# Kernel optimization log

Hardware: AMD Instinct MI355X
Metric: run time of the kernel (lower is better)

The kernel has to match this reference:

```python
import jax, jax.numpy as jnp
import numpy as np

B, S, D = 4, 2048, 768   # batch, seq_len, dim_inp
H, E = 12, 64            # num_heads, dim_out (per-head)
LN_EPS = 1e-5


def setup_inputs() -> dict:
    key = jax.random.key(0)
    ks = jax.random.split(key, 12)
    sd = 1.0 / np.sqrt(D)
    x = jax.random.normal(ks[0], (B, S, D), dtype=jnp.float32)
    Wq = jax.random.normal(ks[1], (H, D, E), dtype=jnp.float32) * sd
    bq = jax.random.normal(ks[2], (H, E), dtype=jnp.float32) * 0.02
    Wk = jax.random.normal(ks[3], (H, D, E), dtype=jnp.float32) * sd
    bk = jax.random.normal(ks[4], (H, E), dtype=jnp.float32) * 0.02
    Wv = jax.random.normal(ks[5], (H, D, E), dtype=jnp.float32) * sd
    bv = jax.random.normal(ks[6], (H, E), dtype=jnp.float32) * 0.02
    Wo = jax.random.normal(ks[7], (H * E, D), dtype=jnp.float32) * (1.0 / np.sqrt(H * E))
    bo = jax.random.normal(ks[8], (D,), dtype=jnp.float32) * 0.02
    gamma = jnp.ones((D,), dtype=jnp.float32)
    beta = jnp.zeros((D,), dtype=jnp.float32)
    return {"input_tensor": x, "Wq": Wq, "bq": bq, "Wk": Wk, "bk": bk,
            "Wv": Wv, "bv": bv, "Wo": Wo, "bo": bo, "gamma": gamma, "beta": beta}


def reference(input_tensor, Wq, bq, Wk, bk, Wv, bv, Wo, bo, gamma, beta):
    x = input_tensor  # [B,S,D]
    # all heads at once: [B,H,S,E]
    q = jnp.einsum('bsd,hde->bhse', x, Wq) + bq[None, :, None, :]
    k = jnp.einsum('bsd,hde->bhse', x, Wk) + bk[None, :, None, :]
    v = jnp.einsum('bsd,hde->bhse', x, Wv) + bv[None, :, None, :]
    # NOTE: original divides by sqrt(seq_len) (query.size(1)), not sqrt(head_dim)
    scale = jnp.sqrt(jnp.float32(q.shape[2]))
    scores = jnp.einsum('bhse,bhte->bhst', q, k) / scale  # [B,H,S,S]
    attn = jax.nn.softmax(scores, axis=-1)
    ctx = jnp.einsum('bhst,bhte->bhse', attn, v)          # [B,H,S,E]
    # concat heads along last dim: [B,S,H*E]
    ctx = ctx.transpose(0, 2, 1, 3).reshape(x.shape[0], x.shape[1], -1)
    proj = ctx @ Wo + bo                                   # [B,S,D]
    h = x + proj
    mu = jnp.mean(h, axis=-1, keepdims=True)
    var = jnp.mean(jnp.square(h - mu), axis=-1, keepdims=True)
    y = (h - mu) * jax.lax.rsqrt(var + LN_EPS) * gamma + beta
    return y
```

## Files before the change

kernel.cpp:

```cpp
#include <hip/hip_runtime.h>


typedef __bf16 bf16x8 __attribute__((ext_vector_type(8)));
typedef __bf16 bf16x4 __attribute__((ext_vector_type(4)));
typedef float  f32x4  __attribute__((ext_vector_type(4)));
typedef float  f32x16 __attribute__((ext_vector_type(16)));
typedef unsigned u32x4 __attribute__((ext_vector_type(4)));

#define MFMA16(a,b,c) __builtin_amdgcn_mfma_f32_16x16x32_bf16((a),(b),(c),0,0,0)
#define MFMA32(a,b,c) __builtin_amdgcn_mfma_f32_32x32x16_bf16((a),(b),(c),0,0,0)
#define QSCALE2 (0.022097086912079612f * 1.4426950408889634f)

__device__ __forceinline__ void gload16(const void* g, void* l) {
  __builtin_amdgcn_global_load_lds((const __attribute__((address_space(1))) void*)g,
                                   (__attribute__((address_space(3))) void*)l, 16, 0, 0);
}

__global__ __launch_bounds__(256) void pack_kernel(
    const float* __restrict__ x, const float* __restrict__ Wq,
    const float* __restrict__ Wk, const float* __restrict__ Wv,
    const float* __restrict__ Wo,
    __bf16* __restrict__ xb, __bf16* __restrict__ wqkv, __bf16* __restrict__ wot) {
  int tid = blockIdx.x * 256 + threadIdx.x;
  int nth = gridDim.x * 256;
  for (int i = tid; i < 8192 * 768 / 4; i += nth) {
    float4 v = ((const float4*)x)[i];
    bf16x4 o; o[0] = (__bf16)v.x; o[1] = (__bf16)v.y; o[2] = (__bf16)v.z; o[3] = (__bf16)v.w;
    ((bf16x4*)xb)[i] = o;
  }
  for (int i = tid; i < 3 * 768 * 768; i += nth) {
    int n = i / 768, d = i - n * 768;
    int p = n / 768;
    int wn = n - p * 768;
    int h = wn >> 6, e = wn & 63;
    const float* W = (p == 0) ? Wq : (p == 1) ? Wk : Wv;
    wqkv[i] = (__bf16)W[(h * 768 + d) * 64 + e];
  }
  for (int i = tid; i < 768 * 768; i += nth) {
    int n = i / 768, k = i - n * 768;
    wot[i] = (__bf16)Wo[k * 768 + n];
  }
}

#define GEMM_CORE(A_, Bt_, m0_, n0_)                                              \
  __shared__ __bf16 As[128 * 32];                                                 \
  __shared__ __bf16 Bs[128 * 32];                                                 \
  const int tid = threadIdx.x;                                                    \
  const int w = tid >> 6, lane = tid & 63, ln = lane & 15, hi = lane >> 4;        \
  const int wr = w >> 1, wc = w & 1;                                              \
  f32x4 acc[4][4];                                                                \
  {                                                                               \
    f32x4 z = {0.f, 0.f, 0.f, 0.f};                                               \
    _Pragma("unroll") for (int i = 0; i < 4; ++i)                                 \
      _Pragma("unroll") for (int j = 0; j < 4; ++j) acc[i][j] = z;                \
  }                                                                               \
  {                                                                               \
    const int r0 = tid >> 2, cc = (tid & 3) * 8;                                  \
    const __bf16* ga0 = A_ + (size_t)(m0_ + r0) * 768 + cc;                       \
    const __bf16* ga1 = A_ + (size_t)(m0_ + 64 + r0) * 768 + cc;                  \
    const __bf16* gb0 = Bt_ + (size_t)(n0_ + r0) * 768 + cc;                      \
    const __bf16* gb1 = Bt_ + (size_t)(n0_ + 64 + r0) * 768 + cc;                 \
    __bf16* la0 = &As[w * 512];                                                   \
    __bf16* la1 = &As[2048 + w * 512];                                            \
    __bf16* lb0 = &Bs[w * 512];                                                   \
    __bf16* lb1 = &Bs[2048 + w * 512];                                            \
    for (int kt = 0; kt < 24; ++kt) {                                             \
      const int kk = kt * 32;                                                     \
      gload16(ga0 + kk, la0);                                                     \
      gload16(ga1 + kk, la1);                                                     \
      gload16(gb0 + kk, lb0);                                                     \
      gload16(gb1 + kk, lb1);                                                     \
      __syncthreads();                                                            \
      bf16x8 af[4], bfv[4];                                                       \
      _Pragma("unroll") for (int mt = 0; mt < 4; ++mt)                            \
        af[mt] = *(const bf16x8*)&As[(wr * 64 + mt * 16 + ln) * 32 + hi * 8];     \
      _Pragma("unroll") for (int nt = 0; nt < 4; ++nt)                            \
        bfv[nt] = *(const bf16x8*)&Bs[(wc * 64 + nt * 16 + ln) * 32 + hi * 8];    \
      _Pragma("unroll") for (int mt = 0; mt < 4; ++mt)                            \
        _Pragma("unroll") for (int nt = 0; nt < 4; ++nt)                          \
          acc[mt][nt] = MFMA16(af[mt], bfv[nt], acc[mt][nt]);                     \
      __syncthreads();                                                            \
    }                                                                             \
  }

__global__ __launch_bounds__(256) void gemm_qkv(
    const __bf16* __restrict__ A, const __bf16* __restrict__ Bt,
    const float* __restrict__ bq, const float* __restrict__ bk,
    const float* __restrict__ bv,
    __bf16* __restrict__ qb, __bf16* __restrict__ kb, __bf16* __restrict__ vt) {
  const int lin = blockIdx.y * 18 + blockIdx.x;
  const int swzb = (lin & 7) * 144 + (lin >> 3);
  const int m0 = (swzb / 18) * 128, n0 = (swzb % 18) * 128;
  GEMM_CORE(A, Bt, m0, n0)
  const int p = n0 / 768;
  const float* bias = (p == 0) ? bq : (p == 1) ? bk : bv;
  const float sc = (p == 0) ? QSCALE2 : 1.0f;
#pragma unroll
  for (int nt = 0; nt < 4; ++nt) {
    int n = n0 + wc * 64 + nt * 16 + ln;
    int wn = n - p * 768;
    int h = wn >> 6, e = wn & 63;
    float bb = bias[wn];
#pragma unroll
    for (int mt = 0; mt < 4; ++mt) {
      int mrow = m0 + wr * 64 + mt * 16 + hi * 4;
      int b = mrow >> 11, s0 = mrow & 2047;
      if (p == 2) {
        bf16x4 pk;
#pragma unroll
        for (int r = 0; r < 4; ++r) pk[r] = (__bf16)(acc[mt][nt][r] + bb);
        *(bf16x4*)&vt[(((size_t)b * 12 + h) * 64 + e) * 2048 + s0] = pk;
      } else {
        __bf16* dst = (p == 0) ? qb : kb;
#pragma unroll
        for (int r = 0; r < 4; ++r)
          dst[(((size_t)b * 12 + h) * 2048 + s0 + r) * 64 + e] =
              (__bf16)((acc[mt][nt][r] + bb) * sc);
      }
    }
  }
}

__global__ __launch_bounds__(256) void gemm_proj(
    const __bf16* __restrict__ A, const __bf16* __restrict__ Bt,
    const float* __restrict__ bo, const float* __restrict__ xres,
    float* __restrict__ hout) {
  const int lin = blockIdx.y * 6 + blockIdx.x;
  const int swzb = (lin & 7) * 48 + (lin >> 3);
  const int m0 = (swzb / 6) * 128, n0 = (swzb % 6) * 128;
  GEMM_CORE(A, Bt, m0, n0)
#pragma unroll
  for (int nt = 0; nt < 4; ++nt) {
    int n = n0 + wc * 64 + nt * 16 + ln;
    float bb = bo[n];
#pragma unroll
    for (int mt = 0; mt < 4; ++mt) {
      int mrow = m0 + wr * 64 + mt * 16 + hi * 4;
#pragma unroll
      for (int r = 0; r < 4; ++r) {
        size_t idx = (size_t)(mrow + r) * 768 + n;
        hout[idx] = acc[mt][nt][r] + bb + xres[idx];
      }
    }
  }
}

__global__ __launch_bounds__(256, 3) void attn_kernel(
    const __bf16* __restrict__ qb, const __bf16* __restrict__ kb,
    const __bf16* __restrict__ vt, __bf16* __restrict__ ctx) {
  __shared__ __align__(16) char lds[32768];
  const int tid = threadIdx.x;
  const int w = tid >> 6, lane = tid & 63;
  const int l31 = lane & 31, h = lane >> 5;
  const int bh = blockIdx.x;
  const int q0 = blockIdx.y * 128 + w * 32;

  const int o0 = tid * 16, o1 = o0 + 4096;
  const int r0s = o0 >> 7, cb0 = o0 & 127;
  const int r1s = o1 >> 7, cb1 = o1 & 127;
  const char* kgb = (const char*)(kb + (size_t)bh * 2048 * 64);
  const char* vgb = (const char*)(vt + (size_t)bh * 64 * 2048);
  const char* ksrc0 = kgb + r0s * 128 + (cb0 ^ ((r0s & 7) << 4));
  const char* ksrc1 = kgb + r1s * 128 + (cb1 ^ ((r1s & 7) << 4));
  const char* vsrc0 = vgb + r0s * 4096 + (cb0 ^ ((r0s & 7) << 4));
  const char* vsrc1 = vgb + r1s * 4096 + (cb1 ^ ((r1s & 7) << 4));
  char* kl0 = lds + w * 1024;
  char* vl0 = lds + 16384 + w * 1024;

#define STAGE(t_, b_) do {                                   \
    gload16(ksrc0 + (size_t)(t_) * 8192, kl0 + (b_) * 8192); \
    gload16(ksrc1 + (size_t)(t_) * 8192, kl0 + (b_) * 8192 + 4096); \
    gload16(vsrc0 + (size_t)(t_) * 128,  vl0 + (b_) * 8192); \
    gload16(vsrc1 + (size_t)(t_) * 128,  vl0 + (b_) * 8192 + 4096); \
  } while (0)

  const __bf16* qp = qb + ((size_t)bh * 2048 + q0 + l31) * 64 + h * 8;
  bf16x8 qf[4];
#pragma unroll
  for (int s = 0; s < 4; ++s) qf[s] = *(const bf16x8*)(qp + 16 * s);

  const int swz = (l31 & 7) << 4;
  const int krd = l31 * 128 + ((h * 16) ^ swz);
  const int vrd = 16384 + l31 * 128 + ((h * 16) ^ swz);
  int ka_[8], va_[8];
#pragma unroll
  for (int kvt = 0; kvt < 2; ++kvt)
#pragma unroll
    for (int s = 0; s < 4; ++s) ka_[kvt * 4 + s] = (krd + kvt * 4096) ^ (s * 32);
#pragma unroll
  for (int ks = 0; ks < 4; ++ks)
#pragma unroll
    for (int et = 0; et < 2; ++et) va_[ks * 2 + et] = (vrd + et * 4096) ^ (ks * 32);

  f32x16 FZ;
#pragma unroll
  for (int r = 0; r < 16; ++r) FZ[r] = 0.f;
  bf16x8 onesf;
#pragma unroll
  for (int j = 0; j < 8; ++j) onesf[j] = (__bf16)1.0f;

  f32x16 lacc = FZ;
  f32x16 cacc[2];
  cacc[0] = FZ; cacc[1] = FZ;

  STAGE(0, 0);
  __syncthreads();

#define PKPAIR(dst_, i_)                                                       \
  {                                                                            \
    float pa_ = __builtin_amdgcn_exp2f(sa[2 * (i_)]);                          \
    float pb_ = __builtin_amdgcn_exp2f(sa[2 * (i_) + 1]);                      \
    asm("v_cvt_pk_bf16_f32 %0, %1, %2" : "=v"(dst_) : "v"(pa_), "v"(pb_));     \
  }

#define TILEBODY(B_, T_)                                                       \
  {                                                                            \
    if ((T_) < 31) STAGE((T_) + 1, (B_) ^ 1);                                  \
    bf16x8 kf[2][4], vf[4][2];                                                 \
    _Pragma("unroll") for (int kvt = 0; kvt < 2; ++kvt)                        \
      _Pragma("unroll") for (int s = 0; s < 4; ++s)                            \
        kf[kvt][s] = *(const bf16x8*)(lds + (B_) * 8192 + ka_[kvt * 4 + s]);   \
    _Pragma("unroll") for (int ks = 0; ks < 4; ++ks)                           \
      _Pragma("unroll") for (int et = 0; et < 2; ++et)                         \
        vf[ks][et] = *(const bf16x8*)(lds + (B_) * 8192 + va_[ks * 2 + et]);   \
    u32x4 pau[4];                                                              \
    _Pragma("unroll") for (int kvt = 0; kvt < 2; ++kvt) {                      \
      __builtin_amdgcn_s_setprio(1);                                           \
      f32x16 sa = MFMA32(kf[kvt][0], qf[0], FZ);                               \
      sa = MFMA32(kf[kvt][1], qf[1], sa);                                      \
      sa = MFMA32(kf[kvt][2], qf[2], sa);                                      \
      sa = MFMA32(kf[kvt][3], qf[3], sa);                                      \
      __builtin_amdgcn_s_setprio(0);                                           \
      unsigned c0, c1, c2, c3, c4, c5, c6, c7;                                 \
      PKPAIR(c0, 0) PKPAIR(c1, 1) PKPAIR(c2, 2) PKPAIR(c3, 3)                  \
      PKPAIR(c4, 4) PKPAIR(c5, 5) PKPAIR(c6, 6) PKPAIR(c7, 7)                  \
      asm("v_permlane32_swap_b32 %0, %1" : "+v"(c0), "+v"(c2));                \
      asm("v_permlane32_swap_b32 %0, %1" : "+v"(c1), "+v"(c3));                \
      asm("v_permlane32_swap_b32 %0, %1" : "+v"(c4), "+v"(c6));                \
      asm("v_permlane32_swap_b32 %0, %1" : "+v"(c5), "+v"(c7));                \
      pau[2 * kvt][0] = c0; pau[2 * kvt][1] = c1;                              \
      pau[2 * kvt][2] = c2; pau[2 * kvt][3] = c3;                              \
      pau[2 * kvt + 1][0] = c4; pau[2 * kvt + 1][1] = c5;                      \
      pau[2 * kvt + 1][2] = c6; pau[2 * kvt + 1][3] = c7;                      \
      lacc = MFMA32(__builtin_bit_cast(bf16x8, pau[2 * kvt]), onesf, lacc);    \
      lacc = MFMA32(__builtin_bit_cast(bf16x8, pau[2 * kvt + 1]), onesf, lacc);\
    }                                                                          \
    __builtin_amdgcn_s_setprio(1);                                             \
    _Pragma("unroll") for (int ks = 0; ks < 4; ++ks) {                         \
      bf16x8 paf = __builtin_bit_cast(bf16x8, pau[ks]);                        \
      cacc[0] = MFMA32(paf, vf[ks][0], cacc[0]);                               \
      cacc[1] = MFMA32(paf, vf[ks][1], cacc[1]);                               \
    }                                                                          \
    __builtin_amdgcn_s_setprio(0);                                             \
    __syncthreads();                                                           \
  }

  for (int t = 0; t < 32; t += 2) {
    TILEBODY(0, t)
    TILEBODY(1, t + 1)
  }
#undef TILEBODY
#undef PKPAIR
#undef STAGE

  const int b = bh / 12, hh = bh - b * 12;
#pragma unroll
  for (int r = 0; r < 16; ++r) {
    const int ql = (r & 3) + 8 * (r >> 2) + 4 * h;
    float rl = __builtin_amdgcn_rcpf(lacc[r]);
    size_t base = ((size_t)b * 2048 + q0 + ql) * 768 + hh * 64 + l31;
    ctx[base]      = (__bf16)(cacc[0][r] * rl);
    ctx[base + 32] = (__bf16)(cacc[1][r] * rl);
  }
}

__global__ __launch_bounds__(256) void ln_kernel(
    const float* __restrict__ hb, const float* __restrict__ gamma,
    const float* __restrict__ beta, float* __restrict__ out) {
  __shared__ float ssum[4], ssq[4];
  const int row = blockIdx.x, t = threadIdx.x;
  const float* hr = hb + (size_t)row * 768;
  float v0 = hr[t], v1 = hr[t + 256], v2 = hr[t + 512];
  float sum = v0 + v1 + v2;
  float sq = v0 * v0 + v1 * v1 + v2 * v2;
#pragma unroll
  for (int mask = 1; mask < 64; mask <<= 1) {
    sum += __shfl_xor(sum, mask, 64);
    sq += __shfl_xor(sq, mask, 64);
  }
  const int w = t >> 6;
  if ((t & 63) == 0) { ssum[w] = sum; ssq[w] = sq; }
  __syncthreads();
  float s1 = ssum[0] + ssum[1] + ssum[2] + ssum[3];
  float s2 = ssq[0] + ssq[1] + ssq[2] + ssq[3];
  float mu = s1 * (1.0f / 768.0f);
  float var = s2 * (1.0f / 768.0f) - mu * mu;
  float rs = rsqrtf(var + 1e-5f);
  float* orow = out + (size_t)row * 768;
  orow[t]       = (v0 - mu) * rs * gamma[t]       + beta[t];
  orow[t + 256] = (v1 - mu) * rs * gamma[t + 256] + beta[t + 256];
  orow[t + 512] = (v2 - mu) * rs * gamma[t + 512] + beta[t + 512];
}

extern "C" void kernel_launch(void* const* d_in, const int* in_sizes, int n_in,
                              void* d_out, int out_size, void* d_ws, size_t ws_size,
                              hipStream_t stream) {
  const float* x     = (const float*)d_in[0];
  const float* Wq    = (const float*)d_in[1];
  const float* bq    = (const float*)d_in[2];
  const float* Wk    = (const float*)d_in[3];
  const float* bk    = (const float*)d_in[4];
  const float* Wv    = (const float*)d_in[5];
  const float* bv    = (const float*)d_in[6];
  const float* Wo    = (const float*)d_in[7];
  const float* bo    = (const float*)d_in[8];
  const float* gamma = (const float*)d_in[9];
  const float* beta  = (const float*)d_in[10];
  float* out = (float*)d_out;

  char* ws = (char*)d_ws;
  __bf16* xb   = (__bf16*)(ws);
  __bf16* wqkv = (__bf16*)(ws + 12582912);
  __bf16* wot  = (__bf16*)(ws + 16121856);
  __bf16* qb   = (__bf16*)(ws + 17301504);
  __bf16* kb   = (__bf16*)(ws + 29884416);
  __bf16* vt   = (__bf16*)(ws + 42467328);
  __bf16* ctx  = (__bf16*)(ws + 55050240);
  float*  hb   = (float*)(ws + 67633152);

  pack_kernel<<<dim3(1024), dim3(256), 0, stream>>>(x, Wq, Wk, Wv, Wo, xb, wqkv, wot);
  gemm_qkv<<<dim3(18, 64), dim3(256), 0, stream>>>(xb, wqkv, bq, bk, bv, qb, kb, vt);
  attn_kernel<<<dim3(48, 16), dim3(256), 0, stream>>>(qb, kb, vt, ctx);
  gemm_proj<<<dim3(6, 64), dim3(256), 0, stream>>>(ctx, wot, bo, x, hb);
  ln_kernel<<<dim3(8192), dim3(256), 0, stream>>>(hb, gamma, beta, out);
}
```

Baseline: 166.5 us.

## Software-pipeline PV MFMAs one tile behind QK softmax in attention loop

```diff
diff --git a/kernel.cpp b/kernel.cpp
--- a/kernel.cpp
+++ b/kernel.cpp
@@ -203,6 +203,9 @@
   f32x16 cacc[2];
   cacc[0] = FZ; cacc[1] = FZ;
 
+  u32x4 pauA[4], pauB[4];
+  bf16x8 vfA[4][2], vfB[4][2];
+
   STAGE(0, 0);
   __syncthreads();
 
@@ -213,17 +216,25 @@
     asm("v_cvt_pk_bf16_f32 %0, %1, %2" : "=v"(dst_) : "v"(pa_), "v"(pb_));     \
   }
 
-#define TILEBODY(B_, T_)                                                       \
+#define TILEBODY(BUF_, T_, pauC_, vfC_, pauP_, vfP_, DOPV_)                    \
   {                                                                            \
-    if ((T_) < 31) STAGE((T_) + 1, (B_) ^ 1);                                  \
-    bf16x8 kf[2][4], vf[4][2];                                                 \
+    if ((T_) < 31) STAGE((T_) + 1, (BUF_) ^ 1);                                \
+    bf16x8 kf[2][4];                                                           \
     _Pragma("unroll") for (int kvt = 0; kvt < 2; ++kvt)                        \
       _Pragma("unroll") for (int s = 0; s < 4; ++s)                            \
-        kf[kvt][s] = *(const bf16x8*)(lds + (B_) * 8192 + ka_[kvt * 4 + s]);   \
+        kf[kvt][s] = *(const bf16x8*)(lds + (BUF_) * 8192 + ka_[kvt * 4 + s]); \
     _Pragma("unroll") for (int ks = 0; ks < 4; ++ks)                           \
       _Pragma("unroll") for (int et = 0; et < 2; ++et)                         \
-        vf[ks][et] = *(const bf16x8*)(lds + (B_) * 8192 + va_[ks * 2 + et]);   \
-    u32x4 pau[4];                                                              \
+        vfC_[ks][et] = *(const bf16x8*)(lds + (BUF_) * 8192 + va_[ks * 2 + et]); \
+    if (DOPV_) {                                                               \
+      __builtin_amdgcn_s_setprio(1);                                           \
+      _Pragma("unroll") for (int ks = 0; ks < 4; ++ks) {                       \
+        bf16x8 paf = __builtin_bit_cast(bf16x8, pauP_[ks]);                    \
+        cacc[0] = MFMA32(paf, vfP_[ks][0], cacc[0]);                           \
+        cacc[1] = MFMA32(paf, vfP_[ks][1], cacc[1]);                           \
+      }                                                                        \
+      __builtin_amdgcn_s_setprio(0);                                           \
+    }                                                                          \
     _Pragma("unroll") for (int kvt = 0; kvt < 2; ++kvt) {                      \
       __builtin_amdgcn_s_setprio(1);                                           \
       f32x16 sa = MFMA32(kf[kvt][0], qf[0], FZ);                               \
@@ -238,27 +249,30 @@
       asm("v_permlane32_swap_b32 %0, %1" : "+v"(c1), "+v"(c3));                \
       asm("v_permlane32_swap_b32 %0, %1" : "+v"(c4), "+v"(c6));                \
       asm("v_permlane32_swap_b32 %0, %1" : "+v"(c5), "+v"(c7));                \
-      pau[2 * kvt][0] = c0; pau[2 * kvt][1] = c1;                              \
-      pau[2 * kvt][2] = c2; pau[2 * kvt][3] = c3;                              \
-      pau[2 * kvt + 1][0] = c4; pau[2 * kvt + 1][1] = c5;                      \
-      pau[2 * kvt + 1][2] = c6; pau[2 * kvt + 1][3] = c7;                      \
-      lacc = MFMA32(__builtin_bit_cast(bf16x8, pau[2 * kvt]), onesf, lacc);    \
-      lacc = MFMA32(__builtin_bit_cast(bf16x8, pau[2 * kvt + 1]), onesf, lacc);\
+      pauC_[2 * kvt][0] = c0; pauC_[2 * kvt][1] = c1;                          \
+      pauC_[2 * kvt][2] = c2; pauC_[2 * kvt][3] = c3;                          \
+      pauC_[2 * kvt + 1][0] = c4; pauC_[2 * kvt + 1][1] = c5;                  \
+      pauC_[2 * kvt + 1][2] = c6; pauC_[2 * kvt + 1][3] = c7;                  \
+      lacc = MFMA32(__builtin_bit_cast(bf16x8, pauC_[2 * kvt]), onesf, lacc);  \
+      lacc = MFMA32(__builtin_bit_cast(bf16x8, pauC_[2 * kvt + 1]), onesf, lacc); \
     }                                                                          \
-    __builtin_amdgcn_s_setprio(1);                                             \
-    _Pragma("unroll") for (int ks = 0; ks < 4; ++ks) {                         \
-      bf16x8 paf = __builtin_bit_cast(bf16x8, pau[ks]);                        \
-      cacc[0] = MFMA32(paf, vf[ks][0], cacc[0]);                               \
-      cacc[1] = MFMA32(paf, vf[ks][1], cacc[1]);                               \
-    }                                                                          \
-    __builtin_amdgcn_s_setprio(0);                                             \
     __syncthreads();                                                           \
   }
 
-  for (int t = 0; t < 32; t += 2) {
-    TILEBODY(0, t)
-    TILEBODY(1, t + 1)
-  }
+  TILEBODY(0, 0, pauA, vfA, pauB, vfB, 0)
+  for (int t = 1; t < 31; t += 2) {
+    TILEBODY(1, t, pauB, vfB, pauA, vfA, 1)
+    TILEBODY(0, t + 1, pauA, vfA, pauB, vfB, 1)
+  }
+  TILEBODY(1, 31, pauB, vfB, pauA, vfA, 1)
+  __builtin_amdgcn_s_setprio(1);
+#pragma unroll
+  for (int ks = 0; ks < 4; ++ks) {
+    bf16x8 paf = __builtin_bit_cast(bf16x8, pauB[ks]);
+    cacc[0] = MFMA32(paf, vfB[ks][0], cacc[0]);
+    cacc[1] = MFMA32(paf, vfB[ks][1], cacc[1]);
+  }
+  __builtin_amdgcn_s_setprio(0);
 #undef TILEBODY
 #undef PKPAIR
 #undef STAGE
```

Result: slower. 285.3 us (+71.4%).

## Split attention KV range in two and combine partials in a new kernel

Applied to the files above, without the earlier changes.

```diff
diff --git a/kernel.cpp b/kernel.cpp
--- a/kernel.cpp
+++ b/kernel.cpp
@@ -147,19 +147,22 @@
 
 __global__ __launch_bounds__(256, 3) void attn_kernel(
     const __bf16* __restrict__ qb, const __bf16* __restrict__ kb,
-    const __bf16* __restrict__ vt, __bf16* __restrict__ ctx) {
+    const __bf16* __restrict__ vt, __bf16* __restrict__ pc,
+    float* __restrict__ pl) {
   __shared__ __align__(16) char lds[32768];
   const int tid = threadIdx.x;
   const int w = tid >> 6, lane = tid & 63;
   const int l31 = lane & 31, h = lane >> 5;
   const int bh = blockIdx.x;
-  const int q0 = blockIdx.y * 128 + w * 32;
+  const int yy = blockIdx.y;
+  const int half = yy & 1;
+  const int q0 = (yy >> 1) * 128 + w * 32;
 
   const int o0 = tid * 16, o1 = o0 + 4096;
   const int r0s = o0 >> 7, cb0 = o0 & 127;
   const int r1s = o1 >> 7, cb1 = o1 & 127;
-  const char* kgb = (const char*)(kb + (size_t)bh * 2048 * 64);
-  const char* vgb = (const char*)(vt + (size_t)bh * 64 * 2048);
+  const char* kgb = (const char*)(kb + (size_t)bh * 2048 * 64) + half * 131072;
+  const char* vgb = (const char*)(vt + (size_t)bh * 64 * 2048) + half * 2048;
   const char* ksrc0 = kgb + r0s * 128 + (cb0 ^ ((r0s & 7) << 4));
   const char* ksrc1 = kgb + r1s * 128 + (cb1 ^ ((r1s & 7) << 4));
   const char* vsrc0 = vgb + r0s * 4096 + (cb0 ^ ((r0s & 7) << 4));
@@ -215,7 +218,7 @@
 
 #define TILEBODY(B_, T_)                                                       \
   {                                                                            \
-    if ((T_) < 31) STAGE((T_) + 1, (B_) ^ 1);                                  \
+    if ((T_) < 15) STAGE((T_) + 1, (B_) ^ 1);                                  \
     bf16x8 kf[2][4], vf[4][2];                                                 \
     _Pragma("unroll") for (int kvt = 0; kvt < 2; ++kvt)                        \
       _Pragma("unroll") for (int s = 0; s < 4; ++s)                            \
@@ -255,7 +258,7 @@
     __syncthreads();                                                           \
   }
 
-  for (int t = 0; t < 32; t += 2) {
+  for (int t = 0; t < 16; t += 2) {
     TILEBODY(0, t)
     TILEBODY(1, t + 1)
   }
@@ -263,15 +266,36 @@
 #undef PKPAIR
 #undef STAGE
 
+  __bf16* pcH = pc + (size_t)half * 6291456;
+  float* plH = pl + half * 98304;
   const int b = bh / 12, hh = bh - b * 12;
 #pragma unroll
   for (int r = 0; r < 16; ++r) {
     const int ql = (r & 3) + 8 * (r >> 2) + 4 * h;
-    float rl = __builtin_amdgcn_rcpf(lacc[r]);
     size_t base = ((size_t)b * 2048 + q0 + ql) * 768 + hh * 64 + l31;
-    ctx[base]      = (__bf16)(cacc[0][r] * rl);
-    ctx[base + 32] = (__bf16)(cacc[1][r] * rl);
-  }
+    pcH[base]      = (__bf16)cacc[0][r];
+    pcH[base + 32] = (__bf16)cacc[1][r];
+    if (l31 == 0) plH[bh * 2048 + q0 + ql] = lacc[r];
+  }
+}
+
+__global__ __launch_bounds__(256) void combine_kernel(
+    const __bf16* __restrict__ pc, const float* __restrict__ pl,
+    __bf16* __restrict__ ctx) {
+  const int i = blockIdx.x * 256 + threadIdx.x;
+  const int base = i * 4;
+  const int row = base / 768;
+  const int c = base - row * 768;
+  const int b = row >> 11, q = row & 2047, h = c >> 6;
+  const int lidx = ((b * 12 + h) << 11) + q;
+  const float den = pl[lidx] + pl[98304 + lidx];
+  const float rl = __builtin_amdgcn_rcpf(den);
+  bf16x4 a = *(const bf16x4*)(pc + base);
+  bf16x4 d = *(const bf16x4*)(pc + 6291456 + base);
+  bf16x4 o;
+#pragma unroll
+  for (int j = 0; j < 4; ++j) o[j] = (__bf16)(((float)a[j] + (float)d[j]) * rl);
+  *(bf16x4*)(ctx + base) = o;
 }
 
 __global__ __launch_bounds__(256) void ln_kernel(
@@ -327,10 +351,13 @@
   __bf16* vt   = (__bf16*)(ws + 42467328);
   __bf16* ctx  = (__bf16*)(ws + 55050240);
   float*  hb   = (float*)(ws + 67633152);
+  __bf16* pc   = (__bf16*)(ws + 67633152);
+  float*  pl   = (float*)(ws + 92798976);
 
   pack_kernel<<<dim3(1024), dim3(256), 0, stream>>>(x, Wq, Wk, Wv, Wo, xb, wqkv, wot);
   gemm_qkv<<<dim3(18, 64), dim3(256), 0, stream>>>(xb, wqkv, bq, bk, bv, qb, kb, vt);
-  attn_kernel<<<dim3(48, 16), dim3(256), 0, stream>>>(qb, kb, vt, ctx);
+  attn_kernel<<<dim3(48, 32), dim3(256), 0, stream>>>(qb, kb, vt, pc, pl);
+  combine_kernel<<<dim3(6144), dim3(256), 0, stream>>>(pc, pl, ctx);
   gemm_proj<<<dim3(6, 64), dim3(256), 0, stream>>>(ctx, wot, bo, x, hb);
   ln_kernel<<<dim3(8192), dim3(256), 0, stream>>>(hb, gamma, beta, out);
 }
```

Measured after the change: 177.0 us. 1.06x slower.

## Double GEMM K-tile with XOR-swizzled LDS and store residual pre-LN in bf16

Applied to the files above, without the earlier changes.

```diff
diff --git a/kernel.cpp b/kernel.cpp
--- a/kernel.cpp
+++ b/kernel.cpp
@@ -43,8 +43,8 @@
 }
 
 #define GEMM_CORE(A_, Bt_, m0_, n0_)                                              \
-  __shared__ __bf16 As[128 * 32];                                                 \
-  __shared__ __bf16 Bs[128 * 32];                                                 \
+  __shared__ __align__(16) __bf16 As[128 * 64];                                   \
+  __shared__ __align__(16) __bf16 Bs[128 * 64];                                   \
   const int tid = threadIdx.x;                                                    \
   const int w = tid >> 6, lane = tid & 63, ln = lane & 15, hi = lane >> 4;        \
   const int wr = w >> 1, wc = w & 1;                                              \
@@ -54,31 +54,33 @@
     _Pragma("unroll") for (int i = 0; i < 4; ++i)                                 \
       _Pragma("unroll") for (int j = 0; j < 4; ++j) acc[i][j] = z;                \
   }                                                                               \
+  const int colx0 = ((hi) ^ (ln & 7)) << 4;         \
+  const int colx1 = ((4 + hi) ^ (ln & 7)) << 4;     \
   {                                                                               \
-    const int r0 = tid >> 2, cc = (tid & 3) * 8;                                  \
-    const __bf16* ga0 = A_ + (size_t)(m0_ + r0) * 768 + cc;                       \
-    const __bf16* ga1 = A_ + (size_t)(m0_ + 64 + r0) * 768 + cc;                  \
-    const __bf16* gb0 = Bt_ + (size_t)(n0_ + r0) * 768 + cc;                      \
-    const __bf16* gb1 = Bt_ + (size_t)(n0_ + 64 + r0) * 768 + cc;                 \
-    __bf16* la0 = &As[w * 512];                                                   \
-    __bf16* la1 = &As[2048 + w * 512];                                            \
-    __bf16* lb0 = &Bs[w * 512];                                                   \
-    __bf16* lb1 = &Bs[2048 + w * 512];                                            \
-    for (int kt = 0; kt < 24; ++kt) {                                             \
-      const int kk = kt * 32;                                                     \
-      gload16(ga0 + kk, la0);                                                     \
-      gload16(ga1 + kk, la1);                                                     \
-      gload16(gb0 + kk, lb0);                                                     \
-      gload16(gb1 + kk, lb1);                                                     \
+    const int r0 = tid >> 3;                       \
+    const int scb = ((tid & 7) * 16) ^ ((r0 & 7) << 4);     \
+    const char* gA = (const char*)(A_) + (size_t)(m0_ + r0) * 1536 + scb;         \
+    const char* gB = (const char*)(Bt_) + (size_t)(n0_ + r0) * 1536 + scb;        \
+    char* lA = (char*)As + w * 1024;    \
+    char* lB = (char*)Bs + w * 1024;                                              \
+    for (int kt = 0; kt < 12; ++kt) {                                             \
+      const int kb = kt * 128;                                                    \
+      _Pragma("unroll") for (int j = 0; j < 4; ++j) {                             \
+        gload16(gA + j * 49152 + kb, lA + j * 4096);                              \
+        gload16(gB + j * 49152 + kb, lB + j * 4096);                              \
+      }                                                                           \
       __syncthreads();                                                            \
-      bf16x8 af[4], bfv[4];                                                       \
-      _Pragma("unroll") for (int mt = 0; mt < 4; ++mt)                            \
-        af[mt] = *(const bf16x8*)&As[(wr * 64 + mt * 16 + ln) * 32 + hi * 8];     \
-      _Pragma("unroll") for (int nt = 0; nt < 4; ++nt)                            \
-        bfv[nt] = *(const bf16x8*)&Bs[(wc * 64 + nt * 16 + ln) * 32 + hi * 8];    \
-      _Pragma("unroll") for (int mt = 0; mt < 4; ++mt)                            \
+      _Pragma("unroll") for (int kk = 0; kk < 2; ++kk) {                          \
+        const int cx = kk ? colx1 : colx0;                                        \
+        bf16x8 af[4], bfv[4];                                                     \
+        _Pragma("unroll") for (int mt = 0; mt < 4; ++mt)                          \
+          af[mt] = *(const bf16x8*)((char*)As + (wr * 64 + mt * 16 + ln) * 128 + cx); \
         _Pragma("unroll") for (int nt = 0; nt < 4; ++nt)                          \
-          acc[mt][nt] = MFMA16(af[mt], bfv[nt], acc[mt][nt]);                     \
+          bfv[nt] = *(const bf16x8*)((char*)Bs + (wc * 64 + nt * 16 + ln) * 128 + cx); \
+        _Pragma("unroll") for (int mt = 0; mt < 4; ++mt)                          \
+          _Pragma("unroll") for (int nt = 0; nt < 4; ++nt)                        \
+            acc[mt][nt] = MFMA16(af[mt], bfv[nt], acc[mt][nt]);                   \
+      }                                                                           \
       __syncthreads();                                                            \
     }                                                                             \
   }
@@ -123,8 +125,8 @@
 
 __global__ __launch_bounds__(256) void gemm_proj(
     const __bf16* __restrict__ A, const __bf16* __restrict__ Bt,
-    const float* __restrict__ bo, const float* __restrict__ xres,
-    float* __restrict__ hout) {
+    const float* __restrict__ bo, const __bf16* __restrict__ xres,
+    __bf16* __restrict__ hout) {
   const int lin = blockIdx.y * 6 + blockIdx.x;
   const int swzb = (lin & 7) * 48 + (lin >> 3);
   const int m0 = (swzb / 6) * 128, n0 = (swzb % 6) * 128;
@@ -139,7 +141,7 @@
 #pragma unroll
       for (int r = 0; r < 4; ++r) {
         size_t idx = (size_t)(mrow + r) * 768 + n;
-        hout[idx] = acc[mt][nt][r] + bb + xres[idx];
+        hout[idx] = (__bf16)(acc[mt][nt][r] + bb + (float)xres[idx]);
       }
     }
   }
@@ -275,12 +277,12 @@
 }
 
 __global__ __launch_bounds__(256) void ln_kernel(
-    const float* __restrict__ hb, const float* __restrict__ gamma,
+    const __bf16* __restrict__ hb, const float* __restrict__ gamma,
     const float* __restrict__ beta, float* __restrict__ out) {
   __shared__ float ssum[4], ssq[4];
   const int row = blockIdx.x, t = threadIdx.x;
-  const float* hr = hb + (size_t)row * 768;
-  float v0 = hr[t], v1 = hr[t + 256], v2 = hr[t + 512];
+  const __bf16* hr = hb + (size_t)row * 768;
+  float v0 = (float)hr[t], v1 = (float)hr[t + 256], v2 = (float)hr[t + 512];
   float sum = v0 + v1 + v2;
   float sq = v0 * v0 + v1 * v1 + v2 * v2;
 #pragma unroll
@@ -326,11 +328,11 @@
   __bf16* kb   = (__bf16*)(ws + 29884416);
   __bf16* vt   = (__bf16*)(ws + 42467328);
   __bf16* ctx  = (__bf16*)(ws + 55050240);
-  float*  hb   = (float*)(ws + 67633152);
+  __bf16* hb   = (__bf16*)(ws + 67633152);
 
   pack_kernel<<<dim3(1024), dim3(256), 0, stream>>>(x, Wq, Wk, Wv, Wo, xb, wqkv, wot);
   gemm_qkv<<<dim3(18, 64), dim3(256), 0, stream>>>(xb, wqkv, bq, bk, bv, qb, kb, vt);
   attn_kernel<<<dim3(48, 16), dim3(256), 0, stream>>>(qb, kb, vt, ctx);
-  gemm_proj<<<dim3(6, 64), dim3(256), 0, stream>>>(ctx, wot, bo, x, hb);
+  gemm_proj<<<dim3(6, 64), dim3(256), 0, stream>>>(ctx, wot, bo, xb, hb);
   ln_kernel<<<dim3(8192), dim3(256), 0, stream>>>(hb, gamma, beta, out);
 }
```

Measured after the change: 158.1 us (median of 3 runs). -5.0%, faster.
